# Performance work log

Hardware: AMD Instinct MI355X
Metric: run time of the kernel (lower is better)

## Reference

```python
import jax, jax.numpy as jnp
import numpy as np
from jax import lax

KS = 3            # kernel_size
K = 32            # cluster_num
NB = 32           # num_base_kernels
HID = 64          # mlp_hidden_dim
COUT = 64         # out_channels
MAX_ITER = 20
TOL = 0.005


def _unfold3(x):
    # torch nn.Unfold(k=3, pad=1): output channel order is (c, kh, kw)
    b, c, h, w = x.shape
    xp = jnp.pad(x, ((0, 0), (0, 0), (1, 1), (1, 1)))
    cols = [xp[:, :, i:i + h, j:j + w] for i in range(KS) for j in range(KS)]
    p = jnp.stack(cols, axis=2)  # [B, C, 9, H, W]
    return p.reshape(b, c * KS * KS, h * w).transpose(0, 2, 1)  # [B, HW, C*9]


def _kmeans_single(key, sample):
    # sample: [N, D]. Lloyd iterations with early stop on total center shift.
    n, d = sample.shape
    centers0 = sample[jax.random.permutation(key, n)[:K]]

    def assign(centers):
        d2 = (jnp.sum(sample * sample, 1, keepdims=True)
              - 2.0 * (sample @ centers.T)
              + jnp.sum(centers * centers, 1))
        return jnp.argmin(d2, axis=1)

    def body(carry):
        i, centers, _ = carry
        a = assign(centers)
        oh = jax.nn.one_hot(a, K, dtype=sample.dtype)  # [N, K]
        counts = oh.sum(0)                             # [K]
        sums = oh.T @ sample                           # [K, D]
        new = jnp.where(counts[:, None] > 0,
                        sums / jnp.maximum(counts, 1.0)[:, None],
                        centers)
        shift = jnp.sum(jnp.linalg.norm(new - centers, axis=1))
        return (i + 1, new, shift)

    def cond(carry):
        i, _, shift = carry
        return jnp.logical_and(i < MAX_ITER, shift >= TOL * n)

    init = (jnp.int32(0), centers0, jnp.asarray(jnp.inf, sample.dtype))
    _, centers, _ = lax.while_loop(cond, body, init)
    return assign(centers)


def _kmeans(features):
    keys = jax.random.split(jax.random.key(42), features.shape[0])
    return jax.vmap(_kmeans_single)(keys, features)


def _mlp(x, w1, b1, w2, b2, w3, b3):
    h = jax.nn.relu(x @ w1 + b1)
    h = jax.nn.relu(h @ w2 + b2)
    return h @ w3 + b3


def setup_inputs() -> dict:
    key = jax.random.key(0)
    ks = jax.random.split(key, 16)
    B, C, H, W = 2, 32, 64, 64
    F = C * KS * KS
    fan = 1.0 / np.sqrt(F)
    fanh = 1.0 / np.sqrt(HID)
    return {
        'x': jax.random.normal(ks[0], (B, C, H, W), jnp.float32),
        'base_kernels': jax.random.normal(ks[1], (NB, F, COUT), jnp.float32) * np.sqrt(2.0 / F),
        'kg_w1': jax.random.normal(ks[2], (F, HID), jnp.float32) * fan,
        'kg_b1': jnp.zeros((HID,), jnp.float32),
        'kg_w2': jax.random.normal(ks[3], (HID, HID), jnp.float32) * fanh,
        'kg_b2': jnp.zeros((HID,), jnp.float32),
        'kg_w3': jax.random.normal(ks[4], (HID, NB), jnp.float32) * fanh,
        'kg_b3': jnp.zeros((NB,), jnp.float32),
        'bg_w1': jax.random.normal(ks[5], (F, HID), jnp.float32) * fan,
        'bg_b1': jnp.zeros((HID,), jnp.float32),
        'bg_w2': jax.random.normal(ks[6], (HID, HID), jnp.float32) * fanh,
        'bg_b2': jnp.zeros((HID,), jnp.float32),
        'bg_w3': jax.random.normal(ks[7], (HID, COUT), jnp.float32) * fanh,
        'bg_b3': jnp.zeros((COUT,), jnp.float32),
    }


def reference(x, base_kernels, kg_w1, kg_b1, kg_w2, kg_b2, kg_w3, kg_b3,
              bg_w1, bg_b1, bg_w2, bg_b2, bg_w3, bg_b3):
    B, C, H, W = x.shape
    patches = _unfold3(x)  # [B, P, F] with F = C*9
    P = patches.shape[1]
    # observation features: mean over kernel area per channel
    obs = patches.reshape(B, P, C, KS * KS).mean(-1)  # [B, P, C]
    idx = _kmeans(obs)  # [B, P] int cluster assignments

    # per-cluster centers of the full patch features (scatter-mean)
    oh = jax.nn.one_hot(idx, K, dtype=patches.dtype)          # [B, P, K]
    sums = jnp.einsum('bpk,bpf->bkf', oh, patches)            # [B, K, F]
    counts = jnp.maximum(oh.sum(1), 1.0)                      # [B, K]
    centers = sums / counts[:, :, None]                       # [B, K, F]

    # adaptive kernels = softmax-mixture of base kernels
    attn = jax.nn.softmax(_mlp(centers, kg_w1, kg_b1, kg_w2, kg_b2, kg_w3, kg_b3), axis=-1)  # [B,K,NB]
    kernels = jnp.einsum('bkn,nfc->bkfc', attn, base_kernels)  # [B, K, F, COUT]
    biases = _mlp(centers, bg_w1, bg_b1, bg_w2, bg_b2, bg_w3, bg_b3)  # [B, K, COUT]

    # combine: out[b,p] = patches[b,p] @ kernels[b, idx[b,p]] + biases[b, idx[b,p]]
    bidx = jnp.arange(B)[:, None]
    wtok = kernels[bidx, idx]   # [B, P, F, COUT]
    btok = biases[bidx, idx]    # [B, P, COUT]
    out = jnp.einsum('bpf,bpfc->bpc', patches, wtok) + btok
    out = out.transpose(0, 2, 1).reshape(B, COUT, H, W)
    return (out, idx)
```

## Files before the change

kernel.cpp:

```cpp
#include <hip/hip_runtime.h>
#include <hip/hip_bf16.h>
#include <vector>
#include <algorithm>
#include <utility>
#include <stdint.h>

#define BB 2
#define PP 4096
#define FF 288
#define KK 32
#define NBASE 32
#define HID 64
#define COUT 64
#define NWG_KM 32
#define SUBS 16
#define OUT_ELEMS 524288

#define THREEFRY_PARTITIONABLE 1

typedef unsigned short u16;

#define OFF_IDX    512
#define OFF_ATTN   33280
#define OFF_BIAS   41472
#define OFF_PART   57856
#define OFF_CNTS   320000
#define OFF_CPART  328192
#define OFF_WG     1544704
#define OFF_BAR2   3904000

struct InitIdx { int v[2][32]; };

__device__ __forceinline__ float bf2f(u16 u){
  union { unsigned int i; float f; } cv; cv.i = ((unsigned int)u) << 16; return cv.f;
}
__device__ __forceinline__ u16 f2bf(float f){
  union { float f; unsigned int i; } cv; cv.f = f;
  unsigned int x = cv.i;
  unsigned int r = (x + 0x7FFFu + ((x >> 16) & 1u)) >> 16;
  return (u16)r;
}
__device__ __forceinline__ float u_lo(unsigned int u){
  union { unsigned int i; float f; } cv; cv.i = u << 16; return cv.f;
}
__device__ __forceinline__ float u_hi(unsigned int u){
  union { unsigned int i; float f; } cv; cv.i = u & 0xFFFF0000u; return cv.f;
}

template<bool BF>
__device__ __forceinline__ float ld(const void* p, size_t i){
  if constexpr (BF) { return bf2f(((const u16*)p)[i]); }
  else              { return ((const float*)p)[i]; }
}
template<bool BF>
__device__ __forceinline__ void st(void* p, size_t i, float v){
  if constexpr (BF) { ((u16*)p)[i] = f2bf(v); }
  else              { ((float*)p)[i] = v; }
}

template<bool BF>
__device__ __forceinline__ float obs_chan(const void* x, size_t bi, int h, int w){
  float s = 0.f;
  #pragma unroll
  for (int dh=-1; dh<=1; ++dh){
    int hh = h + dh;
    #pragma unroll
    for (int dw=-1; dw<=1; ++dw){
      int ww = w + dw;
      float v = 0.f;
      if ((unsigned)hh < 64u && (unsigned)ww < 64u) v = ld<BF>(x, bi + (hh<<6) + ww);
      s += v;
    }
  }
  return s / 9.0f;
}

__device__ __forceinline__ void gbar2(int* slots, int* gen, int nwg, int epoch){
  __syncthreads();
  __threadfence();
  const int t = threadIdx.x;
  const int wg = blockIdx.x;
  if (t == 0)
    __hip_atomic_store(&slots[wg*16], epoch, __ATOMIC_RELEASE, __HIP_MEMORY_SCOPE_AGENT);
  if (wg == 0){
    if (t < nwg){
      while (__hip_atomic_load(&slots[t*16], __ATOMIC_ACQUIRE, __HIP_MEMORY_SCOPE_AGENT) < epoch){}
    }
    __syncthreads();
    if (t == 0)
      __hip_atomic_store(gen, epoch, __ATOMIC_RELEASE, __HIP_MEMORY_SCOPE_AGENT);
  }
  if (t == 0){
    while (__hip_atomic_load(gen, __ATOMIC_ACQUIRE, __HIP_MEMORY_SCOPE_AGENT) < epoch){}
  }
  __syncthreads();
  __threadfence();
}

__global__ __launch_bounds__(256) void kDetect(const void* __restrict__ x, int* flag){
  __shared__ int cnt;
  if (threadIdx.x == 0) cnt = 0;
  __syncthreads();
  const u16* p = (const u16*)x;
  int bad = 0;
  for (int i = threadIdx.x; i < 1024; i += 256){
    u16 u = p[2*i];
    unsigned e = (u >> 7) & 0xFFu;
    if (e >= 131u) ++bad;
  }
  atomicAdd(&cnt, bad);
  __syncthreads();
  if (threadIdx.x == 0) *flag = (cnt < 102) ? 1 : 0;
}

template<bool BF>
__device__ void kB_body(const void* __restrict__ x,
                        float* __restrict__ part,
                        float* __restrict__ cnts,
                        int* __restrict__ idxg,
                        void* __restrict__ dout,
                        int* __restrict__ slots,
                        int* __restrict__ gen,
                        const InitIdx& ii,
                        float* obs_st,
                        float* cent,
                        float* cc_s,
                        int*   a_loc,
                        float* sq,
                        float* snorm,
                        float* cntsh,
                        float* acc8,
                        float* cnt8){
  const int t   = threadIdx.x;
  const int wg  = blockIdx.x;
  const int mb  = wg >> 4;
  const int sub = wg & 15;
  const int pg  = sub*256 + t;
  const int d   = t & 31, oct = t >> 5;

  float o[32];
  {
    int h = pg >> 6, w = pg & 63;
    size_t xb = (size_t)mb << 17;
    for (int c=0; c<32; ++c){
      float v = obs_chan<BF>(x, xb + ((size_t)c<<12), h, w);
      o[c] = v; obs_st[t*33 + c] = v;
    }
  }
  if (t < 64){
    int bb = t >> 5, j = t & 31;
    int q = ii.v[bb][j];
    int qh = q >> 6, qw = q & 63;
    size_t xq = (size_t)bb << 17;
    for (int c=0; c<32; ++c) cent[(bb*32 + j)*32 + c] = obs_chan<BF>(x, xq + ((size_t)c<<12), qh, qw);
  }
  __syncthreads();

  float ss = 0.f;
  #pragma unroll
  for (int dd=0; dd<32; ++dd) ss = fmaf(o[dd], o[dd], ss);

  bool act0 = true, act1 = true;
  int parity = 0;

  for (int it=0; it<20; ++it){
    if (!(act0 || act1)) break;
    bool mine = (mb==0) ? act0 : act1;
    if (mine){
      if (t < 32){
        float s = 0.f;
        #pragma unroll
        for (int dd=0; dd<32; ++dd){ float v = cent[(mb*32 + t)*32 + dd]; s = fmaf(v,v,s); }
        cc_s[t] = s;
      }
      __syncthreads();
      float best = 3.0e38f; int bk = 0;
      for (int k=0; k<32; k+=4){
        const float4* c0 = (const float4*)&cent[(mb*32 + k  )*32];
        const float4* c1 = (const float4*)&cent[(mb*32 + k+1)*32];
        const float4* c2 = (const float4*)&cent[(mb*32 + k+2)*32];
        const float4* c3 = (const float4*)&cent[(mb*32 + k+3)*32];
        float dt0=0.f, dt1=0.f, dt2=0.f, dt3=0.f;
        #pragma unroll
        for (int q=0; q<8; ++q){
          float4 a0 = c0[q], a1 = c1[q], a2 = c2[q], a3 = c3[q];
          float o0 = o[q*4+0], o1 = o[q*4+1], o2 = o[q*4+2], o3 = o[q*4+3];
          dt0 = fmaf(o0,a0.x,dt0); dt0 = fmaf(o1,a0.y,dt0); dt0 = fmaf(o2,a0.z,dt0); dt0 = fmaf(o3,a0.w,dt0);
          dt1 = fmaf(o0,a1.x,dt1); dt1 = fmaf(o1,a1.y,dt1); dt1 = fmaf(o2,a1.z,dt1); dt1 = fmaf(o3,a1.w,dt1);
          dt2 = fmaf(o0,a2.x,dt2); dt2 = fmaf(o1,a2.y,dt2); dt2 = fmaf(o2,a2.z,dt2); dt2 = fmaf(o3,a2.w,dt2);
          dt3 = fmaf(o0,a3.x,dt3); dt3 = fmaf(o1,a3.y,dt3); dt3 = fmaf(o2,a3.z,dt3); dt3 = fmaf(o3,a3.w,dt3);
        }
        float di0 = (ss - 2.0f*dt0) + cc_s[k];
        float di1 = (ss - 2.0f*dt1) + cc_s[k+1];
        float di2 = (ss - 2.0f*dt2) + cc_s[k+2];
        float di3 = (ss - 2.0f*dt3) + cc_s[k+3];
        if (di0 < best){ best = di0; bk = k; }
        if (di1 < best){ best = di1; bk = k+1; }
        if (di2 < best){ best = di2; bk = k+2; }
        if (di3 < best){ best = di3; bk = k+3; }
      }
      a_loc[t] = bk;
      __syncthreads();
      for (int e=t; e<8*32*33; e+=256) acc8[e] = 0.f;
      cnt8[t] = 0.f;
      __syncthreads();
      {
        const int p0 = oct*32;
        int kcur = a_loc[p0];
        float racc = 0.f; int rl = 0;
        for (int i=0; i<32; ++i){
          int kp = a_loc[p0+i];
          float v = obs_st[(p0+i)*33 + d];
          if (kp != kcur){
            acc8[(oct*32 + kcur)*33 + d] += racc;
            if (d == 0) cnt8[oct*32 + kcur] += (float)rl;
            racc = 0.f; rl = 0; kcur = kp;
          }
          racc += v; ++rl;
        }
        acc8[(oct*32 + kcur)*33 + d] += racc;
        if (d == 0) cnt8[oct*32 + kcur] += (float)rl;
      }
      __syncthreads();
      float* Pg = part + ((size_t)((parity*2 + mb)*SUBS + sub))*1024;
      {
        float r0=0.f, r1=0.f, r2=0.f, r3=0.f;
        #pragma unroll
        for (int o2=0; o2<8; ++o2){
          r0 += acc8[(o2*32 + oct      )*33 + d];
          r1 += acc8[(o2*32 + oct + 8  )*33 + d];
          r2 += acc8[(o2*32 + oct + 16 )*33 + d];
          r3 += acc8[(o2*32 + oct + 24 )*33 + d];
        }
        Pg[(oct     )*32 + d] = r0;
        Pg[(oct + 8 )*32 + d] = r1;
        Pg[(oct + 16)*32 + d] = r2;
        Pg[(oct + 24)*32 + d] = r3;
      }
      if (t < 32){
        float c = 0.f;
        #pragma unroll
        for (int o2=0; o2<8; ++o2) c += cnt8[o2*32 + t];
        cnts[((size_t)((parity*2 + mb)*SUBS + sub))*32 + t] = c;
      }
    }
    gbar2(slots, gen, NWG_KM, it+1);
    for (int bb=0; bb<2; ++bb){
      bool ab = (bb==0) ? act0 : act1;
      if (!ab) continue;
      const float* Pb = part + (size_t)((parity*2 + bb)*SUBS)*1024;
      const float* Cb = cnts + (size_t)((parity*2 + bb)*SUBS)*32;
      if (t < 32){
        float s = 0.f;
        for (int si=0; si<SUBS; ++si) s += Cb[si*32 + t];
        cntsh[t] = s;
      }
      __syncthreads();
      {
        int k = t >> 3, d4 = (t & 7) * 4;
        float4 v = make_float4(0.f, 0.f, 0.f, 0.f);
        for (int si=0; si<SUBS; ++si){
          const float4 p4 = *(const float4*)&Pb[si*1024 + k*32 + d4];
          v.x += p4.x; v.y += p4.y; v.z += p4.z; v.w += p4.w;
        }
        float cn = cntsh[k];
        float den = fmaxf(cn, 1.f);
        bool pos = cn > 0.f;
        float o0 = cent[(bb*32 + k)*32 + d4+0], o1 = cent[(bb*32 + k)*32 + d4+1];
        float o2 = cent[(bb*32 + k)*32 + d4+2], o3 = cent[(bb*32 + k)*32 + d4+3];
        float n0 = pos ? (v.x / den) : o0;
        float n1 = pos ? (v.y / den) : o1;
        float n2 = pos ? (v.z / den) : o2;
        float n3 = pos ? (v.w / den) : o3;
        float e0 = n0-o0, e1 = n1-o1, e2 = n2-o2, e3 = n3-o3;
        sq[k*32 + d4+0] = e0*e0; sq[k*32 + d4+1] = e1*e1;
        sq[k*32 + d4+2] = e2*e2; sq[k*32 + d4+3] = e3*e3;
        cent[(bb*32 + k)*32 + d4+0] = n0; cent[(bb*32 + k)*32 + d4+1] = n1;
        cent[(bb*32 + k)*32 + d4+2] = n2; cent[(bb*32 + k)*32 + d4+3] = n3;
      }
      __syncthreads();
      if (t < 32){
        float s = 0.f;
        #pragma unroll
        for (int dd=0; dd<32; ++dd) s += sq[t*32 + dd];
        snorm[t] = sqrtf(s);
      }
      __syncthreads();
      float sh = 0.f;
      for (int k=0;k<32;++k) sh += snorm[k];
      bool na = ((it+1) < 20) && ((double)sh >= 20.48);
      if (bb==0) act0 = na; else act1 = na;
      __syncthreads();
    }
    parity ^= 1;
  }
  __syncthreads();
  if (t < 32){
    float s = 0.f;
    #pragma unroll
    for (int dd=0; dd<32; ++dd){ float v = cent[(mb*32 + t)*32 + dd]; s = fmaf(v,v,s); }
    cc_s[t] = s;
  }
  __syncthreads();
  float best = 3.0e38f; int bk = 0;
  for (int k=0; k<32; k+=4){
    const float4* c0 = (const float4*)&cent[(mb*32 + k  )*32];
    const float4* c1 = (const float4*)&cent[(mb*32 + k+1)*32];
    const float4* c2 = (const float4*)&cent[(mb*32 + k+2)*32];
    const float4* c3 = (const float4*)&cent[(mb*32 + k+3)*32];
    float dt0=0.f, dt1=0.f, dt2=0.f, dt3=0.f;
    #pragma unroll
    for (int q=0; q<8; ++q){
      float4 a0 = c0[q], a1 = c1[q], a2 = c2[q], a3 = c3[q];
      float o0 = o[q*4+0], o1 = o[q*4+1], o2 = o[q*4+2], o3 = o[q*4+3];
      dt0 = fmaf(o0,a0.x,dt0); dt0 = fmaf(o1,a0.y,dt0); dt0 = fmaf(o2,a0.z,dt0); dt0 = fmaf(o3,a0.w,dt0);
      dt1 = fmaf(o0,a1.x,dt1); dt1 = fmaf(o1,a1.y,dt1); dt1 = fmaf(o2,a1.z,dt1); dt1 = fmaf(o3,a1.w,dt1);
      dt2 = fmaf(o0,a2.x,dt2); dt2 = fmaf(o1,a2.y,dt2); dt2 = fmaf(o2,a2.z,dt2); dt2 = fmaf(o3,a2.w,dt2);
      dt3 = fmaf(o0,a3.x,dt3); dt3 = fmaf(o1,a3.y,dt3); dt3 = fmaf(o2,a3.z,dt3); dt3 = fmaf(o3,a3.w,dt3);
    }
    float di0 = (ss - 2.0f*dt0) + cc_s[k];
    float di1 = (ss - 2.0f*dt1) + cc_s[k+1];
    float di2 = (ss - 2.0f*dt2) + cc_s[k+2];
    float di3 = (ss - 2.0f*dt3) + cc_s[k+3];
    if (di0 < best){ best = di0; bk = k; }
    if (di1 < best){ best = di1; bk = k+1; }
    if (di2 < best){ best = di2; bk = k+2; }
    if (di3 < best){ best = di3; bk = k+3; }
  }
  idxg[mb*PP + pg] = bk;
  st<BF>(dout, (size_t)OUT_ELEMS + mb*PP + pg, (float)bk);
}

__global__ __launch_bounds__(256) void kB(const void* x, float* part, float* cnts,
                                          int* idxg, void* dout,
                                          int* slots, int* gen,
                                          const int* flag, InitIdx ii){
  __shared__ __align__(16) float obs_st[256*33];
  __shared__ __align__(16) float cent[2*32*32];
  __shared__ float cc_s[32];
  __shared__ int   a_loc[256];
  __shared__ float sq[32*32];
  __shared__ float snorm[32];
  __shared__ float cntsh[32];
  __shared__ float acc8[8*32*33];
  __shared__ float cnt8[8*32];
  if (*flag) kB_body<true >(x, part, cnts, idxg, dout, slots, gen, ii,
                            obs_st, cent, cc_s, a_loc, sq, snorm, cntsh, acc8, cnt8);
  else       kB_body<false>(x, part, cnts, idxg, dout, slots, gen, ii,
                            obs_st, cent, cc_s, a_loc, sq, snorm, cntsh, acc8, cnt8);
}

template<bool BF>
__device__ void kC_body(const void* __restrict__ x,
                        const int* __restrict__ idxg,
                        float* __restrict__ cpartJ,
                        float* __restrict__ acc,
                        int* __restrict__ idxsh){
  int wgid = blockIdx.x;
  int cg = wgid / 9, j = wgid % 9;
  int b = cg >> 4, pc = cg & 15;
  int t = threadIdx.x;
  for (int e=t; e<32*33; e+=256) acc[e] = 0.f;
  idxsh[t] = idxg[b*PP + pc*256 + t];
  __syncthreads();

  int dh = j/3 - 1, dw = j%3 - 1;
  int gp = (pc << 8) + t;
  int h = gp >> 6, w = gp & 63;
  int k = idxsh[t];
  int hh = h + dh, ww = w + dw;
  bool ok = ((unsigned)hh < 64u) && ((unsigned)ww < 64u);
  size_t boff = ((size_t)b << 17) + (hh << 6) + ww;

  #pragma unroll 4
  for (int c=0; c<32; ++c){
    float v = ok ? ld<BF>(x, boff + ((size_t)c << 12)) : 0.f;
    atomicAdd(&acc[k*33 + c], v);
  }
  if (j == 0) atomicAdd(&acc[k*33 + 32], 1.0f);
  __syncthreads();
  float* cp = cpartJ + (size_t)wgid*(32*33);
  for (int e=t; e<32*33; e+=256) cp[e] = acc[e];
}

__global__ __launch_bounds__(256) void kC(const void* x, const int* idxg,
                                          float* cpartJ, const int* flag){
  __shared__ float acc[32*33];
  __shared__ int   idxsh[256];
  if (*flag) kC_body<true >(x, idxg, cpartJ, acc, idxsh);
  else       kC_body<false>(x, idxg, cpartJ, acc, idxsh);
}

template<bool BF>
__device__ void kD_body(const float* __restrict__ cpartJ,
                        const void* kg_w1, const void* kg_b1,
                        const void* kg_w2, const void* kg_b2,
                        const void* kg_w3, const void* kg_b3,
                        const void* bg_w1, const void* bg_b1,
                        const void* bg_w2, const void* bg_b2,
                        const void* bg_w3, const void* bg_b3,
                        float* __restrict__ attn,
                        float* __restrict__ biasO,
                        float* __restrict__ row,
                        float* __restrict__ h1,
                        float* __restrict__ h2,
                        float* __restrict__ lgs){
  int wg = blockIdx.x; int b = wg >> 5; int k = wg & 31;
  int t = threadIdx.x;
  float cnt = 0.f;
  for (int ch=0; ch<16; ++ch)
    cnt += cpartJ[(size_t)((b*16+ch)*9)*(32*33) + k*33 + 32];
  float den = fmaxf(cnt, 1.f);
  for (int f=t; f<FF; f+=64){
    int c = f / 9, j = f % 9;
    float s = 0.f;
    for (int ch=0; ch<16; ++ch)
      s += cpartJ[(size_t)((b*16+ch)*9 + j)*(32*33) + k*33 + c];
    row[f] = s / den;
  }
  __syncthreads();

  {
    float s = 0.f;
    #pragma unroll 8
    for (int f=0; f<FF; ++f) s = fmaf(row[f], ld<BF>(kg_w1, f*HID + t), s);
    h1[t] = fmaxf(s + ld<BF>(kg_b1, t), 0.f);
  }
  __syncthreads();
  {
    float s = 0.f;
    #pragma unroll 8
    for (int h=0; h<HID; ++h) s = fmaf(h1[h], ld<BF>(kg_w2, h*HID + t), s);
    h2[t] = fmaxf(s + ld<BF>(kg_b2, t), 0.f);
  }
  __syncthreads();
  if (t < 32){
    float s = 0.f;
    #pragma unroll 8
    for (int h=0; h<HID; ++h) s = fmaf(h2[h], ld<BF>(kg_w3, h*NBASE + t), s);
    lgs[t] = s + ld<BF>(kg_b3, t);
  }
  __syncthreads();
  if (t < 32){
    float mx = -3.0e38f;
    for (int i=0;i<NBASE;++i) mx = fmaxf(mx, lgs[i]);
    float se = 0.f;
    for (int i=0;i<NBASE;++i) se += expf(lgs[i]-mx);
    attn[wg*NBASE + t] = expf(lgs[t]-mx) / se;
  }
  __syncthreads();
  {
    float s = 0.f;
    #pragma unroll 8
    for (int f=0; f<FF; ++f) s = fmaf(row[f], ld<BF>(bg_w1, f*HID + t), s);
    h1[t] = fmaxf(s + ld<BF>(bg_b1, t), 0.f);
  }
  __syncthreads();
  {
    float s = 0.f;
    #pragma unroll 8
    for (int h=0; h<HID; ++h) s = fmaf(h1[h], ld<BF>(bg_w2, h*HID + t), s);
    h2[t] = fmaxf(s + ld<BF>(bg_b2, t), 0.f);
  }
  __syncthreads();
  {
    float s = 0.f;
    #pragma unroll 8
    for (int h=0; h<HID; ++h) s = fmaf(h2[h], ld<BF>(bg_w3, h*COUT + t), s);
    biasO[wg*COUT + t] = s + ld<BF>(bg_b3, t);
  }
}

__global__ __launch_bounds__(64) void kD(const float* cpartJ,
                                         const void* kg_w1, const void* kg_b1,
                                         const void* kg_w2, const void* kg_b2,
                                         const void* kg_w3, const void* kg_b3,
                                         const void* bg_w1, const void* bg_b1,
                                         const void* bg_w2, const void* bg_b2,
                                         const void* bg_w3, const void* bg_b3,
                                         float* attn, float* biasO, const int* flag){
  __shared__ float row[FF];
  __shared__ float h1[64];
  __shared__ float h2[64];
  __shared__ float lgs[32];
  if (*flag) kD_body<true >(cpartJ, kg_w1,kg_b1,kg_w2,kg_b2,kg_w3,kg_b3,
                            bg_w1,bg_b1,bg_w2,bg_b2,bg_w3,bg_b3, attn, biasO, row,h1,h2,lgs);
  else       kD_body<false>(cpartJ, kg_w1,kg_b1,kg_w2,kg_b2,kg_w3,kg_b3,
                            bg_w1,bg_b1,bg_w2,bg_b2,bg_w3,bg_b3, attn, biasO, row,h1,h2,lgs);
}

template<bool BF>
__device__ void kE_body(const void* __restrict__ base,
                        const float* __restrict__ attn,
                        u16* __restrict__ Wg,
                        float* __restrict__ at,
                        float* __restrict__ tile){
  int wg = blockIdx.x;
  int fq = wg & 3, bk = wg >> 2;
  int t = threadIdx.x;
  if (t < 32) at[t] = attn[bk*NBASE + t];
  __syncthreads();
  int f0 = fq*72;
  for (int e=t; e<72*64; e+=256){
    int fl = e >> 6, c = e & 63;
    size_t bi = (size_t)(f0 + fl)*COUT + c;
    float s = 0.f;
    #pragma unroll 8
    for (int n=0; n<NBASE; ++n)
      s = fmaf(at[n], ld<BF>(base, bi + (size_t)n*FF*COUT), s);
    tile[fl*65 + c] = s;
  }
  __syncthreads();
  for (int e=t; e<72*64; e+=256){
    int c = e / 72, fl = e % 72;
    Wg[(size_t)bk*(64*FF) + (size_t)c*FF + f0 + fl] = f2bf(tile[fl*65 + c]);
  }
}

__global__ __launch_bounds__(256) void kE(const void* base, const float* attn,
                                          u16* Wg, const int* flag){
  __shared__ float at[32];
  __shared__ float tile[72*65];
  if (*flag) kE_body<true >(base, attn, Wg, at, tile);
  else       kE_body<false>(base, attn, Wg, at, tile);
}

template<bool BF>
__device__ void kF_body(const void* __restrict__ x,
                        const int* __restrict__ idxg,
                        const u16* __restrict__ Wg,
                        const float* __restrict__ biasO,
                        void* __restrict__ dout,
                        u16* __restrict__ patch,
                        float* __restrict__ outT){
  int wg = blockIdx.x;
  int q = wg & 3, h = (wg >> 2) & 63, b = wg >> 8;
  int t = threadIdx.x, wv = t >> 6, lane = t & 63;
  int w0 = q << 4;

  for (int e=t; e<16*FF; e+=256){
    int pl = e & 15, fe = e >> 4;
    int c = fe / 9, j = fe % 9;
    int hh = h + j/3 - 1, ww = w0 + pl + (j%3) - 1;
    float v = 0.f;
    if ((unsigned)hh < 64u && (unsigned)ww < 64u)
      v = ld<BF>(x, ((size_t)b << 17) + ((size_t)c << 12) + (hh<<6) + ww);
    patch[pl*296 + fe] = f2bf(v);
  }
  __syncthreads();

  #pragma unroll
  for (int i=0; i<4; ++i){
    int pl = (wv << 2) + i;
    int p = (h << 6) + w0 + pl;
    int k = idxg[(b << 12) + p];
    const uint4* Wp = (const uint4*)(Wg + ((size_t)((b << 5) + k)*64 + lane)*FF);
    const uint4* Pp = (const uint4*)(patch + pl*296);
    float acc = 0.f;
    #pragma unroll 6
    for (int j=0; j<36; ++j){
      uint4 wv4 = Wp[j];
      uint4 pv4 = Pp[j];
      acc = fmaf(u_lo(pv4.x), u_lo(wv4.x), acc);
      acc = fmaf(u_hi(pv4.x), u_hi(wv4.x), acc);
      acc = fmaf(u_lo(pv4.y), u_lo(wv4.y), acc);
      acc = fmaf(u_hi(pv4.y), u_hi(wv4.y), acc);
      acc = fmaf(u_lo(pv4.z), u_lo(wv4.z), acc);
      acc = fmaf(u_hi(pv4.z), u_hi(wv4.z), acc);
      acc = fmaf(u_lo(pv4.w), u_lo(wv4.w), acc);
      acc = fmaf(u_hi(pv4.w), u_hi(wv4.w), acc);
    }
    float bias = biasO[((b << 5) + k)*COUT + lane];
    outT[lane*17 + pl] = acc + bias;
  }
  __syncthreads();

  for (int e=t; e<1024; e+=256){
    int cout = e >> 4, pl = e & 15;
    st<BF>(dout, (((size_t)(b << 6) + cout) << 12) + (h << 6) + w0 + pl,
           outT[cout*17 + pl]);
  }
}

__global__ __launch_bounds__(256) void kF(const void* x, const int* idxg,
                                          const u16* Wg, const float* biasO,
                                          void* dout, const int* flag){
  __shared__ u16   patch[16*296];
  __shared__ float outT[64*17];
  if (*flag) kF_body<true >(x, idxg, Wg, biasO, dout, patch, outT);
  else       kF_body<false>(x, idxg, Wg, biasO, dout, patch, outT);
}

static inline uint32_t rotl32(uint32_t x, int d){ return (x<<d)|(x>>(32-d)); }
static void tf_block(uint32_t k0,uint32_t k1,uint32_t x0,uint32_t x1,uint32_t&o0,uint32_t&o1){
  uint32_t ks2 = k0 ^ k1 ^ 0x1BD11BDAu;
  uint32_t v0 = x0 + k0, v1 = x1 + k1;
  const int ra[4]={13,15,26,6}, rb[4]={17,29,16,24};
  #define R4(r) for(int i_=0;i_<4;++i_){ v0 += v1; v1 = rotl32(v1,(r)[i_]); v1 ^= v0; }
  R4(ra); v0 += k1;  v1 += ks2 + 1u;
  R4(rb); v0 += ks2; v1 += k0  + 2u;
  R4(ra); v0 += k0;  v1 += k1  + 3u;
  R4(rb); v0 += k1;  v1 += ks2 + 4u;
  R4(ra); v0 += ks2; v1 += k0  + 5u;
  #undef R4
  o0 = v0; o1 = v1;
}
struct KP{ uint32_t a, b; };
static void tf_split(KP k, KP& first, KP& second){
#if THREEFRY_PARTITIONABLE
  uint32_t a0,b0,a1,b1;
  tf_block(k.a,k.b, 0u,0u, a0,b0);
  tf_block(k.a,k.b, 0u,1u, a1,b1);
  first  = KP{a0,b0};
  second = KP{a1,b1};
#else
  uint32_t a0,b0,a1,b1;
  tf_block(k.a,k.b, 0u,2u, a0,b0);
  tf_block(k.a,k.b, 1u,3u, a1,b1);
  first  = KP{a0,a1};
  second = KP{b0,b1};
#endif
}
static void random_bits_4096(KP k, std::vector<uint32_t>& bits){
#if THREEFRY_PARTITIONABLE
  for (int i=0;i<4096;++i){
    uint32_t o0,o1; tf_block(k.a,k.b, 0u,(uint32_t)i, o0,o1);
    bits[i] = o0 ^ o1;
  }
#else
  for (int i=0;i<2048;++i){
    uint32_t o0,o1; tf_block(k.a,k.b,(uint32_t)i,(uint32_t)(i+2048),o0,o1);
    bits[i] = o0; bits[i+2048] = o1;
  }
#endif
}
static void perm_first32(KP key, int* out32){
  std::vector<int> vals(4096);
  for (int i=0;i<4096;++i) vals[i] = i;
  std::vector<uint32_t> bits(4096);
  std::vector<std::pair<uint32_t,int>> pr(4096);
  KP k = key;
  for (int r=0;r<2;++r){
    KP nk, sk; tf_split(k, nk, sk); k = nk;
    random_bits_4096(sk, bits);
    for (int i=0;i<4096;++i) pr[i] = std::make_pair(bits[i], vals[i]);
    std::stable_sort(pr.begin(), pr.end(),
        [](const std::pair<uint32_t,int>& a, const std::pair<uint32_t,int>& c){ return a.first < c.first; });
    for (int i=0;i<4096;++i) vals[i] = pr[i].second;
  }
  for (int j=0;j<32;++j) out32[j] = vals[j];
}

extern "C" void kernel_launch(void* const* d_in, const int* in_sizes, int n_in,
                              void* d_out, int out_size, void* d_ws, size_t ws_size,
                              hipStream_t stream) {
  const void* x     = d_in[0];
  const void* base  = d_in[1];
  const void* kg_w1 = d_in[2];
  const void* kg_b1 = d_in[3];
  const void* kg_w2 = d_in[4];
  const void* kg_b2 = d_in[5];
  const void* kg_w3 = d_in[6];
  const void* kg_b3 = d_in[7];
  const void* bg_w1 = d_in[8];
  const void* bg_b1 = d_in[9];
  const void* bg_w2 = d_in[10];
  const void* bg_b2 = d_in[11];
  const void* bg_w3 = d_in[12];
  const void* bg_b3 = d_in[13];

  char* ws = (char*)d_ws;
  int*   flag  = (int*)(ws + 64);
  int*   idxg  = (int*)(ws + OFF_IDX);
  float* attn  = (float*)(ws + OFF_ATTN);
  float* biasO = (float*)(ws + OFF_BIAS);
  float* part  = (float*)(ws + OFF_PART);
  float* cnts  = (float*)(ws + OFF_CNTS);
  float* cpartJ= (float*)(ws + OFF_CPART);
  u16*   Wg    = (u16*)(ws + OFF_WG);
  int*   slots = (int*)(ws + OFF_BAR2);
  int*   gen   = (int*)(ws + OFF_BAR2 + 2048);

  InitIdx ii;
  KP root = KP{0u, 42u};
  KP kb0, kb1; tf_split(root, kb0, kb1);
  perm_first32(kb0, ii.v[0]);
  perm_first32(kb1, ii.v[1]);

  hipMemsetAsync(ws + OFF_BAR2, 0, 4096, stream);

  kDetect<<<1, 256, 0, stream>>>(x, flag);
  kB<<<NWG_KM, 256, 0, stream>>>(x, part, cnts, idxg, d_out, slots, gen, flag, ii);
  kC<<<288, 256, 0, stream>>>(x, idxg, cpartJ, flag);
  kD<<<64, 64, 0, stream>>>(cpartJ,
                            kg_w1, kg_b1, kg_w2, kg_b2, kg_w3, kg_b3,
                            bg_w1, bg_b1, bg_w2, bg_b2, bg_w3, bg_b3,
                            attn, biasO, flag);
  kE<<<256, 256, 0, stream>>>(base, attn, Wg, flag);
  kF<<<512, 256, 0, stream>>>(x, idxg, Wg, biasO, d_out, flag);
}
```

Baseline: 299.2 us.

## Decouple k-means batches with per-batch 16-WG barriers and drop memset launch

The global 32-workgroup barrier is replaced by a flat per-batch barrier in which each workgroup polls only the 16 slots of its own batch. Each batch now iterates independently and stops at its own convergence, and each workgroup updates only its own batch's centers. This removes the redundant center update for the other batch, the two-level gather/broadcast barrier latency, and coupling to the slower-converging batch. The barrier-slot reset is folded into kDetect, so the separate hipMemsetAsync is no longer needed, and workgroups mark their slot with a max value on exit so peers still waiting do not deadlock.

```diff
diff --git a/kernel.cpp b/kernel.cpp
--- a/kernel.cpp
+++ b/kernel.cpp
@@ -75,31 +75,24 @@
   return s / 9.0f;
 }
 
-__device__ __forceinline__ void gbar2(int* slots, int* gen, int nwg, int epoch){
+__device__ __forceinline__ void gbar16(int* slots, int mb, int sub, int epoch){
   __syncthreads();
   __threadfence();
   const int t = threadIdx.x;
-  const int wg = blockIdx.x;
   if (t == 0)
-    __hip_atomic_store(&slots[wg*16], epoch, __ATOMIC_RELEASE, __HIP_MEMORY_SCOPE_AGENT);
-  if (wg == 0){
-    if (t < nwg){
-      while (__hip_atomic_load(&slots[t*16], __ATOMIC_ACQUIRE, __HIP_MEMORY_SCOPE_AGENT) < epoch){}
-    }
-    __syncthreads();
-    if (t == 0)
-      __hip_atomic_store(gen, epoch, __ATOMIC_RELEASE, __HIP_MEMORY_SCOPE_AGENT);
-  }
-  if (t == 0){
-    while (__hip_atomic_load(gen, __ATOMIC_ACQUIRE, __HIP_MEMORY_SCOPE_AGENT) < epoch){}
+    __hip_atomic_store(&slots[(mb*16 + sub)*16], epoch, __ATOMIC_RELEASE, __HIP_MEMORY_SCOPE_AGENT);
+  if (t < 16){
+    while (__hip_atomic_load(&slots[(mb*16 + t)*16], __ATOMIC_ACQUIRE, __HIP_MEMORY_SCOPE_AGENT) < epoch){}
   }
   __syncthreads();
   __threadfence();
 }
 
-__global__ __launch_bounds__(256) void kDetect(const void* __restrict__ x, int* flag){
+__global__ __launch_bounds__(256) void kDetect(const void* __restrict__ x, int* flag,
+                                               int* slots){
   __shared__ int cnt;
   if (threadIdx.x == 0) cnt = 0;
+  for (int i = threadIdx.x; i < 512; i += 256) slots[i] = 0;
   __syncthreads();
   const u16* p = (const u16*)x;
   int bad = 0;
@@ -120,7 +113,6 @@
                         int* __restrict__ idxg,
                         void* __restrict__ dout,
                         int* __restrict__ slots,
-                        int* __restrict__ gen,
                         const InitIdx& ii,
                         float* obs_st,
                         float* cent,
@@ -147,12 +139,11 @@
       o[c] = v; obs_st[t*33 + c] = v;
     }
   }
-  if (t < 64){
-    int bb = t >> 5, j = t & 31;
-    int q = ii.v[bb][j];
+  if (t < 32){
+    int q = ii.v[mb][t];
     int qh = q >> 6, qw = q & 63;
-    size_t xq = (size_t)bb << 17;
-    for (int c=0; c<32; ++c) cent[(bb*32 + j)*32 + c] = obs_chan<BF>(x, xq + ((size_t)c<<12), qh, qw);
+    size_t xq = (size_t)mb << 17;
+    for (int c=0; c<32; ++c) cent[t*32 + c] = obs_chan<BF>(x, xq + ((size_t)c<<12), qh, qw);
   }
   __syncthreads();
 
@@ -160,96 +151,90 @@
   #pragma unroll
   for (int dd=0; dd<32; ++dd) ss = fmaf(o[dd], o[dd], ss);
 
-  bool act0 = true, act1 = true;
+  bool act = true;
   int parity = 0;
 
-  for (int it=0; it<20; ++it){
-    if (!(act0 || act1)) break;
-    bool mine = (mb==0) ? act0 : act1;
-    if (mine){
-      if (t < 32){
-        float s = 0.f;
-        #pragma unroll
-        for (int dd=0; dd<32; ++dd){ float v = cent[(mb*32 + t)*32 + dd]; s = fmaf(v,v,s); }
-        cc_s[t] = s;
+  for (int it=0; it<20 && act; ++it){
+    if (t < 32){
+      float s = 0.f;
+      #pragma unroll
+      for (int dd=0; dd<32; ++dd){ float v = cent[t*32 + dd]; s = fmaf(v,v,s); }
+      cc_s[t] = s;
+    }
+    __syncthreads();
+    float best = 3.0e38f; int bk = 0;
+    for (int k=0; k<32; k+=4){
+      const float4* c0 = (const float4*)&cent[(k  )*32];
+      const float4* c1 = (const float4*)&cent[(k+1)*32];
+      const float4* c2 = (const float4*)&cent[(k+2)*32];
+      const float4* c3 = (const float4*)&cent[(k+3)*32];
+      float dt0=0.f, dt1=0.f, dt2=0.f, dt3=0.f;
+      #pragma unroll
+      for (int q=0; q<8; ++q){
+        float4 a0 = c0[q], a1 = c1[q], a2 = c2[q], a3 = c3[q];
+        float o0 = o[q*4+0], o1 = o[q*4+1], o2 = o[q*4+2], o3 = o[q*4+3];
+        dt0 = fmaf(o0,a0.x,dt0); dt0 = fmaf(o1,a0.y,dt0); dt0 = fmaf(o2,a0.z,dt0); dt0 = fmaf(o3,a0.w,dt0);
+        dt1 = fmaf(o0,a1.x,dt1); dt1 = fmaf(o1,a1.y,dt1); dt1 = fmaf(o2,a1.z,dt1); dt1 = fmaf(o3,a1.w,dt1);
+        dt2 = fmaf(o0,a2.x,dt2); dt2 = fmaf(o1,a2.y,dt2); dt2 = fmaf(o2,a2.z,dt2); dt2 = fmaf(o3,a2.w,dt2);
+        dt3 = fmaf(o0,a3.x,dt3); dt3 = fmaf(o1,a3.y,dt3); dt3 = fmaf(o2,a3.z,dt3); dt3 = fmaf(o3,a3.w,dt3);
       }
-      __syncthreads();
-      float best = 3.0e38f; int bk = 0;
-      for (int k=0; k<32; k+=4){
-        const float4* c0 = (const float4*)&cent[(mb*32 + k  )*32];
-        const float4* c1 = (const float4*)&cent[(mb*32 + k+1)*32];
-        const float4* c2 = (const float4*)&cent[(mb*32 + k+2)*32];
-        const float4* c3 = (const float4*)&cent[(mb*32 + k+3)*32];
-        float dt0=0.f, dt1=0.f, dt2=0.f, dt3=0.f;
-        #pragma unroll
-        for (int q=0; q<8; ++q){
-          float4 a0 = c0[q], a1 = c1[q], a2 = c2[q], a3 = c3[q];
-          float o0 = o[q*4+0], o1 = o[q*4+1], o2 = o[q*4+2], o3 = o[q*4+3];
-          dt0 = fmaf(o0,a0.x,dt0); dt0 = fmaf(o1,a0.y,dt0); dt0 = fmaf(o2,a0.z,dt0); dt0 = fmaf(o3,a0.w,dt0);
-          dt1 = fmaf(o0,a1.x,dt1); dt1 = fmaf(o1,a1.y,dt1); dt1 = fmaf(o2,a1.z,dt1); dt1 = fmaf(o3,a1.w,dt1);
-          dt2 = fmaf(o0,a2.x,dt2); dt2 = fmaf(o1,a2.y,dt2); dt2 = fmaf(o2,a2.z,dt2); dt2 = fmaf(o3,a2.w,dt2);
-          dt3 = fmaf(o0,a3.x,dt3); dt3 = fmaf(o1,a3.y,dt3); dt3 = fmaf(o2,a3.z,dt3); dt3 = fmaf(o3,a3.w,dt3);
+      float di0 = (ss - 2.0f*dt0) + cc_s[k];
+      float di1 = (ss - 2.0f*dt1) + cc_s[k+1];
+      float di2 = (ss - 2.0f*dt2) + cc_s[k+2];
+      float di3 = (ss - 2.0f*dt3) + cc_s[k+3];
+      if (di0 < best){ best = di0; bk = k; }
+      if (di1 < best){ best = di1; bk = k+1; }
+      if (di2 < best){ best = di2; bk = k+2; }
+      if (di3 < best){ best = di3; bk = k+3; }
+    }
+    a_loc[t] = bk;
+    __syncthreads();
+    for (int e=t; e<8*32*33; e+=256) acc8[e] = 0.f;
+    cnt8[t] = 0.f;
+    __syncthreads();
+    {
+      const int p0 = oct*32;
+      int kcur = a_loc[p0];
+      float racc = 0.f; int rl = 0;
+      for (int i=0; i<32; ++i){
+        int kp = a_loc[p0+i];
+        float v = obs_st[(p0+i)*33 + d];
+        if (kp != kcur){
+          acc8[(oct*32 + kcur)*33 + d] += racc;
+          if (d == 0) cnt8[oct*32 + kcur] += (float)rl;
+          racc = 0.f; rl = 0; kcur = kp;
         }
-        float di0 = (ss - 2.0f*dt0) + cc_s[k];
-        float di1 = (ss - 2.0f*dt1) + cc_s[k+1];
-        float di2 = (ss - 2.0f*dt2) + cc_s[k+2];
-        float di3 = (ss - 2.0f*dt3) + cc_s[k+3];
-        if (di0 < best){ best = di0; bk = k; }
-        if (di1 < best){ best = di1; bk = k+1; }
-        if (di2 < best){ best = di2; bk = k+2; }
-        if (di3 < best){ best = di3; bk = k+3; }
+        racc += v; ++rl;
       }
-      a_loc[t] = bk;
-      __syncthreads();
-      for (int e=t; e<8*32*33; e+=256) acc8[e] = 0.f;
-      cnt8[t] = 0.f;
-      __syncthreads();
-      {
-        const int p0 = oct*32;
-        int kcur = a_loc[p0];
-        float racc = 0.f; int rl = 0;
-        for (int i=0; i<32; ++i){
-          int kp = a_loc[p0+i];
-          float v = obs_st[(p0+i)*33 + d];
-          if (kp != kcur){
-            acc8[(oct*32 + kcur)*33 + d] += racc;
-            if (d == 0) cnt8[oct*32 + kcur] += (float)rl;
-            racc = 0.f; rl = 0; kcur = kp;
-          }
-          racc += v; ++rl;
-        }
-        acc8[(oct*32 + kcur)*33 + d] += racc;
-        if (d == 0) cnt8[oct*32 + kcur] += (float)rl;
+      acc8[(oct*32 + kcur)*33 + d] += racc;
+      if (d == 0) cnt8[oct*32 + kcur] += (float)rl;
+    }
+    __syncthreads();
+    float* Pg = part + ((size_t)((parity*2 + mb)*SUBS + sub))*1024;
+    {
+      float r0=0.f, r1=0.f, r2=0.f, r3=0.f;
+      #pragma unroll
+      for (int o2=0; o2<8; ++o2){
+        r0 += acc8[(o2*32 + oct      )*33 + d];
+        r1 += acc8[(o2*32 + oct + 8  )*33 + d];
+        r2 += acc8[(o2*32 + oct + 16 )*33 + d];
+        r3 += acc8[(o2*32 + oct + 24 )*33 + d];
       }
-      __syncthreads();
-      float* Pg = part + ((size_t)((parity*2 + mb)*SUBS + sub))*1024;
-      {
-        float r0=0.f, r1=0.f, r2=0.f, r3=0.f;
-        #pragma unroll
-        for (int o2=0; o2<8; ++o2){
-          r0 += acc8[(o2*32 + oct      )*33 + d];
-          r1 += acc8[(o2*32 + oct + 8  )*33 + d];
-          r2 += acc8[(o2*32 + oct + 16 )*33 + d];
-          r3 += acc8[(o2*32 + oct + 24 )*33 + d];
-        }
-        Pg[(oct     )*32 + d] = r0;
-        Pg[(oct + 8 )*32 + d] = r1;
-        Pg[(oct + 16)*32 + d] = r2;
-        Pg[(oct + 24)*32 + d] = r3;
-      }
-      if (t < 32){
-        float c = 0.f;
-        #pragma unroll
-        for (int o2=0; o2<8; ++o2) c += cnt8[o2*32 + t];
-        cnts[((size_t)((parity*2 + mb)*SUBS + sub))*32 + t] = c;
-      }
-    }
-    gbar2(slots, gen, NWG_KM, it+1);
-    for (int bb=0; bb<2; ++bb){
-      bool ab = (bb==0) ? act0 : act1;
-      if (!ab) continue;
-      const float* Pb = part + (size_t)((parity*2 + bb)*SUBS)*1024;
-      const float* Cb = cnts + (size_t)((parity*2 + bb)*SUBS)*32;
+      Pg[(oct     )*32 + d] = r0;
+      Pg[(oct + 8 )*32 + d] = r1;
+      Pg[(oct + 16)*32 + d] = r2;
+      Pg[(oct + 24)*32 + d] = r3;
+    }
+    if (t < 32){
+      float c = 0.f;
+      #pragma unroll
+      for (int o2=0; o2<8; ++o2) c += cnt8[o2*32 + t];
+      cnts[((size_t)((parity*2 + mb)*SUBS + sub))*32 + t] = c;
+    }
+    gbar16(slots, mb, sub, it+1);
+    {
+      const float* Pb = part + (size_t)((parity*2 + mb)*SUBS)*1024;
+      const float* Cb = cnts + (size_t)((parity*2 + mb)*SUBS)*32;
       if (t < 32){
         float s = 0.f;
         for (int si=0; si<SUBS; ++si) s += Cb[si*32 + t];
@@ -266,8 +251,8 @@
         float cn = cntsh[k];
         float den = fmaxf(cn, 1.f);
         bool pos = cn > 0.f;
-        float o0 = cent[(bb*32 + k)*32 + d4+0], o1 = cent[(bb*32 + k)*32 + d4+1];
-        float o2 = cent[(bb*32 + k)*32 + d4+2], o3 = cent[(bb*32 + k)*32 + d4+3];
+        float o0 = cent[k*32 + d4+0], o1 = cent[k*32 + d4+1];
+        float o2 = cent[k*32 + d4+2], o3 = cent[k*32 + d4+3];
         float n0 = pos ? (v.x / den) : o0;
         float n1 = pos ? (v.y / den) : o1;
         float n2 = pos ? (v.z / den) : o2;
@@ -275,8 +260,8 @@
         float e0 = n0-o0, e1 = n1-o1, e2 = n2-o2, e3 = n3-o3;
         sq[k*32 + d4+0] = e0*e0; sq[k*32 + d4+1] = e1*e1;
         sq[k*32 + d4+2] = e2*e2; sq[k*32 + d4+3] = e3*e3;
-        cent[(bb*32 + k)*32 + d4+0] = n0; cent[(bb*32 + k)*32 + d4+1] = n1;
-        cent[(bb*32 + k)*32 + d4+2] = n2; cent[(bb*32 + k)*32 + d4+3] = n3;
+        cent[k*32 + d4+0] = n0; cent[k*32 + d4+1] = n1;
+        cent[k*32 + d4+2] = n2; cent[k*32 + d4+3] = n3;
       }
       __syncthreads();
       if (t < 32){
@@ -288,26 +273,27 @@
       __syncthreads();
       float sh = 0.f;
       for (int k=0;k<32;++k) sh += snorm[k];
-      bool na = ((it+1) < 20) && ((double)sh >= 20.48);
-      if (bb==0) act0 = na; else act1 = na;
+      act = ((it+1) < 20) && ((double)sh >= 20.48);
       __syncthreads();
     }
     parity ^= 1;
   }
+  if (t == 0)
+    __hip_atomic_store(&slots[(mb*16 + sub)*16], 0x7FFFFFFF, __ATOMIC_RELEASE, __HIP_MEMORY_SCOPE_AGENT);
   __syncthreads();
   if (t < 32){
     float s = 0.f;
     #pragma unroll
-    for (int dd=0; dd<32; ++dd){ float v = cent[(mb*32 + t)*32 + dd]; s = fmaf(v,v,s); }
+    for (int dd=0; dd<32; ++dd){ float v = cent[t*32 + dd]; s = fmaf(v,v,s); }
     cc_s[t] = s;
   }
   __syncthreads();
   float best = 3.0e38f; int bk = 0;
   for (int k=0; k<32; k+=4){
-    const float4* c0 = (const float4*)&cent[(mb*32 + k  )*32];
-    const float4* c1 = (const float4*)&cent[(mb*32 + k+1)*32];
-    const float4* c2 = (const float4*)&cent[(mb*32 + k+2)*32];
-    const float4* c3 = (const float4*)&cent[(mb*32 + k+3)*32];
+    const float4* c0 = (const float4*)&cent[(k  )*32];
+    const float4* c1 = (const float4*)&cent[(k+1)*32];
+    const float4* c2 = (const float4*)&cent[(k+2)*32];
+    const float4* c3 = (const float4*)&cent[(k+3)*32];
     float dt0=0.f, dt1=0.f, dt2=0.f, dt3=0.f;
     #pragma unroll
     for (int q=0; q<8; ++q){
@@ -333,10 +319,10 @@
 
 __global__ __launch_bounds__(256) void kB(const void* x, float* part, float* cnts,
                                           int* idxg, void* dout,
-                                          int* slots, int* gen,
+                                          int* slots,
                                           const int* flag, InitIdx ii){
   __shared__ __align__(16) float obs_st[256*33];
-  __shared__ __align__(16) float cent[2*32*32];
+  __shared__ __align__(16) float cent[32*32];
   __shared__ float cc_s[32];
   __shared__ int   a_loc[256];
   __shared__ float sq[32*32];
@@ -344,9 +330,9 @@
   __shared__ float cntsh[32];
   __shared__ float acc8[8*32*33];
   __shared__ float cnt8[8*32];
-  if (*flag) kB_body<true >(x, part, cnts, idxg, dout, slots, gen, ii,
+  if (*flag) kB_body<true >(x, part, cnts, idxg, dout, slots, ii,
                             obs_st, cent, cc_s, a_loc, sq, snorm, cntsh, acc8, cnt8);
-  else       kB_body<false>(x, part, cnts, idxg, dout, slots, gen, ii,
+  else       kB_body<false>(x, part, cnts, idxg, dout, slots, ii,
                             obs_st, cent, cc_s, a_loc, sq, snorm, cntsh, acc8, cnt8);
 }
 
@@ -679,7 +665,6 @@
   float* cpartJ= (float*)(ws + OFF_CPART);
   u16*   Wg    = (u16*)(ws + OFF_WG);
   int*   slots = (int*)(ws + OFF_BAR2);
-  int*   gen   = (int*)(ws + OFF_BAR2 + 2048);
 
   InitIdx ii;
   KP root = KP{0u, 42u};
@@ -687,10 +672,8 @@
   perm_first32(kb0, ii.v[0]);
   perm_first32(kb1, ii.v[1]);
 
-  hipMemsetAsync(ws + OFF_BAR2, 0, 4096, stream);
-
-  kDetect<<<1, 256, 0, stream>>>(x, flag);
-  kB<<<NWG_KM, 256, 0, stream>>>(x, part, cnts, idxg, d_out, slots, gen, flag, ii);
+  kDetect<<<1, 256, 0, stream>>>(x, flag, slots);
+  kB<<<NWG_KM, 256, 0, stream>>>(x, part, cnts, idxg, d_out, slots, flag, ii);
   kC<<<288, 256, 0, stream>>>(x, idxg, cpartJ, flag);
   kD<<<64, 64, 0, stream>>>(cpartJ,
                             kg_w1, kg_b1, kg_w2, kg_b2, kg_w3, kg_b3,
```

New measurement: 292.2 us. 1.02x faster.
